# Optimization experiments

Hardware: AMD Instinct MI355X
Metric: run time of the kernel (lower is better)

Reference implementation:

```python
import jax, jax.numpy as jnp
import numpy as np

B, D, U, C = 2048, 512, 512, 100


def setup_inputs() -> dict:
    key = jax.random.key(0)
    k1, k2, k3 = jax.random.split(key, 3)
    x = jax.random.normal(k1, (B, D), dtype=jnp.float32)
    classes = jax.random.randint(k2, (B, 1), 0, C, dtype=jnp.int64)
    # glorot-uniform-like init for the per-class kernel table
    limit = np.sqrt(6.0 / (D + U)).astype(np.float32)
    kernel = jax.random.uniform(k3, (C, D, U), dtype=jnp.float32, minval=-limit, maxval=limit)
    bias = jnp.zeros((C, U), dtype=jnp.float32)
    return {"x": x, "classes": classes, "kernel": kernel, "bias": bias}


def reference(x, classes, kernel, bias):
    cls = jnp.squeeze(classes, axis=1)            # [B]
    w = kernel[cls]                               # [B, D, U] per-sample gathered kernel
    out = jnp.einsum('bd,bdu->bu', x, w)          # batched matmul, x treated as [B,1,D]
    out = out + bias[cls]                         # per-sample gathered bias
    return out                                    # activation is None (linear)
```

## Files before the change

### kernel.cpp

```cpp
#include <hip/hip_runtime.h>
#include <hip/hip_bf16.h>


typedef __attribute__((ext_vector_type(8))) short bf16x8;
typedef __attribute__((ext_vector_type(4))) short short4v;
typedef __attribute__((ext_vector_type(4))) float floatx4;

constexpr int C_CLS   = 100;
constexpr int B_N     = 2048;
constexpr int D_DIM   = 512;
constexpr int U_DIM   = 512;
constexpr int S_CHUNK = 16;
constexpr int MAX_CHUNKS = 228;
constexpr int TU      = 256;
constexpr int PROWS   = 16;
constexpr int PIECES  = D_DIM / PROWS;
constexpr int NWG     = 2 * MAX_CHUNKS;

__device__ __forceinline__ short f2bf(float f) {
    return (short)__builtin_bit_cast(unsigned short, __float2bfloat16(f));
}


__global__ void k_sort(const int* __restrict__ cls, int* __restrict__ order,
                       int* __restrict__ total_chunks, int* __restrict__ chunk_cls,
                       int* __restrict__ chunk_start, int* __restrict__ chunk_len) {
    __shared__ int s_cnt[128], s_off[128], s_chk[128], s_cur[128], s_base[128];
    int tid = threadIdx.x;
    if (tid < 128) s_cnt[tid] = 0;
    __syncthreads();
    for (int i = tid; i < B_N; i += 1024) atomicAdd(&s_cnt[cls[i]], 1);
    __syncthreads();
    int cnt = 0, nch = 0;
    if (tid < 128) {
        cnt = (tid < C_CLS) ? s_cnt[tid] : 0;
        nch = (cnt + S_CHUNK - 1) / S_CHUNK;
        s_off[tid] = cnt; s_chk[tid] = nch;
    }
    __syncthreads();
    for (int st = 1; st < 128; st <<= 1) {
        int a = 0, b = 0;
        if (tid >= st && tid < 128) { a = s_off[tid - st]; b = s_chk[tid - st]; }
        __syncthreads();
        if (tid < 128) { s_off[tid] += a; s_chk[tid] += b; }
        __syncthreads();
    }
    if (tid < C_CLS) {
        int off = s_off[tid] - cnt;
        int cb  = s_chk[tid] - nch;
        s_base[tid] = off;
        s_cur[tid]  = 0;
        for (int j = 0; j < nch; ++j) {
            chunk_cls[cb + j]   = tid;
            chunk_start[cb + j] = off + j * S_CHUNK;
            chunk_len[cb + j]   = min(S_CHUNK, cnt - j * S_CHUNK);
        }
    }
    if (tid == 127) *total_chunks = s_chk[127];
    __syncthreads();
    for (int i = tid; i < B_N; i += 1024) {
        int c = cls[i];
        int p = atomicAdd(&s_cur[c], 1);
        order[s_base[c] + p] = i;
    }
}


#define ISSUE(pi, qq) do {                                                    \
    const int db_ = (pi) * PROWS;                                             \
    _Pragma("unroll")                                                         \
    for (int j_ = 0; j_ < 4; ++j_) {                                          \
        const int r_ = 4 * wv + j_;                                           \
        const float* gp_ = Wg + (size_t)(db_ + r_) * U_DIM + ((lane ^ r_) << 2); \
        __builtin_amdgcn_global_load_lds(                                     \
            (const __attribute__((address_space(1))) void*)gp_,               \
            (__attribute__((address_space(3))) void*)&wbuf[qq][r_][0],        \
            16, 0, 0);                                                        \
    }                                                                         \
} while (0)

#define COMPUTE(pi, qq) do {                                                  \
    const char* xp_ = (const char*)xsb + sA * 1024 +                          \
                      (((pi) * 32 + g4 * 8) ^ sxw_);                          \
    short4v a4 = *reinterpret_cast<const short4v*>(xp_);                      \
    bf16x8 a8;                                                                \
    a8[0] = a4[0]; a8[1] = a4[1]; a8[2] = a4[2]; a8[3] = a4[3];               \
    a8[4] = a4[0]; a8[5] = a4[1]; a8[6] = a4[2]; a8[7] = a4[3];               \
    const char* wb_ = (const char*)wbuf + (qq) * (PROWS * TU * 4);            \
    _Pragma("unroll")                                                         \
    for (int nt = 0; nt < 4; ++nt) {                                          \
        const int cb4_ = ((wv << 6) + nt * 16 + sA) << 2;                     \
        bf16x8 b8;                                                            \
        _Pragma("unroll")                                                     \
        for (int j_ = 0; j_ < 4; ++j_) {                                      \
            const int rl_ = g4 * 4 + j_;                                      \
            float w_ = *reinterpret_cast<const float*>(                       \
                wb_ + rl_ * 1024 + (cb4_ ^ (rl_ << 4)));                      \
            b8[j_] = f2bf(w_);                                                \
        }                                                                     \
        b8[4] = 0; b8[5] = 0; b8[6] = 0; b8[7] = 0;                           \
        acc[nt] = __builtin_amdgcn_mfma_f32_16x16x32_bf16(a8, b8, acc[nt], 0, 0, 0); \
    }                                                                         \
} while (0)

__launch_bounds__(256, 2)
__global__ void k_main(const float* __restrict__ x, const float* __restrict__ kern,
                       const float* __restrict__ bias, const int* __restrict__ order,
                       const int* __restrict__ total_chunks,
                       const int* __restrict__ chunk_cls,
                       const int* __restrict__ chunk_start,
                       const int* __restrict__ chunk_len,
                       float* __restrict__ out) {
    int tc = *total_chunks;
    int A  = 2 * tc;
    int xc = blockIdx.x & 7;
    int ii = blockIdx.x >> 3;
    int q  = A >> 3, r = A & 7;
    int mycnt = (xc < r) ? (q + 1) : q;
    if (ii >= mycnt) return;
    int g = ((xc < r) ? xc * (q + 1) : r * (q + 1) + (xc - r) * q) + ii;

    int chunk = g >> 1;
    int ytile = g & 1;

    int tid  = threadIdx.x;
    int lane = tid & 63;
    int wv   = tid >> 6;
    int sA   = lane & 15;
    int g4   = lane >> 4;
    const int sxw_ = (sA & 7) << 4;

    int c     = chunk_cls[chunk];
    int start = chunk_start[chunk];
    int len   = chunk_len[chunk];
    int u0    = ytile * TU;

    __shared__ float          wbuf[2][PROWS][TU];
    __shared__ unsigned short xsb[S_CHUNK][D_DIM];
    __shared__ int            sidx[S_CHUNK];

    const float* Wg = kern + (size_t)c * (D_DIM * U_DIM) + u0;

    if (tid < S_CHUNK) sidx[tid] = (tid < len) ? order[start + tid] : -1;
    asm volatile("s_waitcnt lgkmcnt(0)" ::: "memory");
    __builtin_amdgcn_s_barrier();

    int srow = tid >> 4;
    int cb   = (tid & 15) * 32;
    int bsmp = sidx[srow]; if (bsmp < 0) bsmp = sidx[0];
    float4 xv[8];
    #pragma unroll
    for (int j = 0; j < 8; ++j)
        xv[j] = reinterpret_cast<const float4*>(x + (size_t)bsmp * D_DIM + cb)[j];

    ISSUE(0, 0);
    ISSUE(1, 1);
    asm volatile("s_waitcnt vmcnt(8)" ::: "memory");

    {
        char* xrow = (char*)xsb + srow * 1024;
        int   swz  = (srow & 7) << 4;
        #pragma unroll
        for (int m = 0; m < 4; ++m) {
            bf16x8 pk;
            pk[0] = f2bf(xv[2*m].x);   pk[1] = f2bf(xv[2*m].y);
            pk[2] = f2bf(xv[2*m].z);   pk[3] = f2bf(xv[2*m].w);
            pk[4] = f2bf(xv[2*m+1].x); pk[5] = f2bf(xv[2*m+1].y);
            pk[6] = f2bf(xv[2*m+1].z); pk[7] = f2bf(xv[2*m+1].w);
            *reinterpret_cast<bf16x8*>(xrow + ((cb * 2 + m * 16) ^ swz)) = pk;
        }
    }
    asm volatile("s_waitcnt lgkmcnt(0)" ::: "memory");
    __builtin_amdgcn_s_barrier();

    floatx4 acc[4];
    #pragma unroll
    for (int k = 0; k < 4; ++k) acc[k] = (floatx4){0.f, 0.f, 0.f, 0.f};

    #pragma unroll 1
    for (int i = 0; i < PIECES; ++i) {
        if (i + 1 < PIECES) asm volatile("s_waitcnt vmcnt(4)" ::: "memory");
        else                asm volatile("s_waitcnt vmcnt(0)" ::: "memory");
        __builtin_amdgcn_s_barrier();
        COMPUTE(i, (i & 1));
        asm volatile("" ::: "memory");
        __builtin_amdgcn_s_barrier();
        if (i + 2 < PIECES) ISSUE(i + 2, (i & 1));
    }

    #pragma unroll
    for (int nt = 0; nt < 4; ++nt) {
        int u = u0 + (wv << 6) + nt * 16 + sA;
        float bb = bias[c * U_DIM + u];
        #pragma unroll
        for (int r2 = 0; r2 < 4; ++r2) {
            int b = sidx[g4 * 4 + r2];
            if (b >= 0) out[(size_t)b * U_DIM + u] = acc[nt][r2] + bb;
        }
    }
}


extern "C" void kernel_launch(void* const* d_in, const int* in_sizes, int n_in,
                              void* d_out, int out_size, void* d_ws, size_t ws_size,
                              hipStream_t stream) {
    const float* x    = (const float*)d_in[0];
    const int*   cls  = (const int*)d_in[1];
    const float* kern = (const float*)d_in[2];
    const float* bias = (const float*)d_in[3];
    float*       out  = (float*)d_out;

    int* ws           = (int*)d_ws;
    int* order        = ws;
    int* total_chunks = ws + 2048;
    int* chunk_cls    = ws + 2112;
    int* chunk_start  = ws + 2368;
    int* chunk_len    = ws + 2624;

    hipLaunchKernelGGL(k_sort, dim3(1), dim3(1024), 0, stream,
                       cls, order, total_chunks, chunk_cls, chunk_start, chunk_len);
    hipLaunchKernelGGL(k_main, dim3(NWG), dim3(256), 0, stream,
                       x, kern, bias, order, total_chunks, chunk_cls, chunk_start, chunk_len, out);
}
```

Before: 38.76 us.

## Use 32-sample chunks with 128-wide U tiles and 4-deep LDS pipeline

Doubles samples per chunk to 32 so each kernel tile loaded from memory feeds two MFMA row-blocks, and halves the U tile to 128 so there are four tiles per chunk. The weight prefetch ring grows from 2 to 4 stages with explicit vmcnt waits unrolled at the tail. The aim is to cut redundant kernel-table reads for classes with more than 16 samples and to hide more load latency. In exchange, small classes waste more padded rows, and the extra x rows are loaded per workgroup.

```diff
diff --git a/kernel.cpp b/kernel.cpp
--- a/kernel.cpp
+++ b/kernel.cpp
@@ -10,12 +10,13 @@
 constexpr int B_N     = 2048;
 constexpr int D_DIM   = 512;
 constexpr int U_DIM   = 512;
-constexpr int S_CHUNK = 16;
-constexpr int MAX_CHUNKS = 228;
-constexpr int TU      = 256;
+constexpr int S_CHUNK = 32;
+constexpr int MAX_CHUNKS = 164;
+constexpr int TU      = 128;
 constexpr int PROWS   = 16;
 constexpr int PIECES  = D_DIM / PROWS;
-constexpr int NWG     = 2 * MAX_CHUNKS;
+constexpr int NQ      = 4;
+constexpr int NWG     = 4 * MAX_CHUNKS;
 
 __device__ __forceinline__ short f2bf(float f) {
     return (short)__builtin_bit_cast(unsigned short, __float2bfloat16(f));
@@ -69,9 +70,11 @@
 #define ISSUE(pi, qq) do {                                                    \
     const int db_ = (pi) * PROWS;                                             \
     _Pragma("unroll")                                                         \
-    for (int j_ = 0; j_ < 4; ++j_) {                                          \
-        const int r_ = 4 * wv + j_;                                           \
-        const float* gp_ = Wg + (size_t)(db_ + r_) * U_DIM + ((lane ^ r_) << 2); \
+    for (int j_ = 0; j_ < 2; ++j_) {                                          \
+        const int r_  = wv * 4 + 2 * j_;           \
+        const int rr_ = r_ + (lane >> 5);        \
+        const float* gp_ = Wg + (size_t)(db_ + rr_) * U_DIM                   \
+                           + (((lane & 31) ^ (rr_ & 15)) << 2);               \
         __builtin_amdgcn_global_load_lds(                                     \
             (const __attribute__((address_space(1))) void*)gp_,               \
             (__attribute__((address_space(3))) void*)&wbuf[qq][r_][0],        \
@@ -80,27 +83,43 @@
 } while (0)
 
 #define COMPUTE(pi, qq) do {                                                  \
-    const char* xp_ = (const char*)xsb + sA * 1024 +                          \
-                      (((pi) * 32 + g4 * 8) ^ sxw_);                          \
-    short4v a4 = *reinterpret_cast<const short4v*>(xp_);                      \
-    bf16x8 a8;                                                                \
-    a8[0] = a4[0]; a8[1] = a4[1]; a8[2] = a4[2]; a8[3] = a4[3];               \
-    a8[4] = a4[0]; a8[5] = a4[1]; a8[6] = a4[2]; a8[7] = a4[3];               \
+    bf16x8 a8_0, a8_1;                                                        \
+    {                                                                         \
+        const int xb_ = ((pi) * 32 + g4 * 8) ^ sxw_;                          \
+        short4v a4 = *reinterpret_cast<const short4v*>(                       \
+            (const char*)xsb + sA * 1024 + xb_);                              \
+        a8_0[0]=a4[0]; a8_0[1]=a4[1]; a8_0[2]=a4[2]; a8_0[3]=a4[3];           \
+        a8_0[4]=a4[0]; a8_0[5]=a4[1]; a8_0[6]=a4[2]; a8_0[7]=a4[3];           \
+        short4v a4b = *reinterpret_cast<const short4v*>(                      \
+            (const char*)xsb + (16 + sA) * 1024 + xb_);                       \
+        a8_1[0]=a4b[0]; a8_1[1]=a4b[1]; a8_1[2]=a4b[2]; a8_1[3]=a4b[3];       \
+        a8_1[4]=a4b[0]; a8_1[5]=a4b[1]; a8_1[6]=a4b[2]; a8_1[7]=a4b[3];       \
+    }                                                                         \
     const char* wb_ = (const char*)wbuf + (qq) * (PROWS * TU * 4);            \
     _Pragma("unroll")                                                         \
-    for (int nt = 0; nt < 4; ++nt) {                                          \
-        const int cb4_ = ((wv << 6) + nt * 16 + sA) << 2;                     \
+    for (int nt = 0; nt < 2; ++nt) {                                          \
+        const int cb4_ = ((wv << 5) + nt * 16 + sA) << 2;                     \
         bf16x8 b8;                                                            \
         _Pragma("unroll")                                                     \
         for (int j_ = 0; j_ < 4; ++j_) {                                      \
             const int rl_ = g4 * 4 + j_;                                      \
             float w_ = *reinterpret_cast<const float*>(                       \
-                wb_ + rl_ * 1024 + (cb4_ ^ (rl_ << 4)));                      \
+                wb_ + rl_ * 512 + (cb4_ ^ (rl_ << 4)));                       \
             b8[j_] = f2bf(w_);                                                \
         }                                                                     \
         b8[4] = 0; b8[5] = 0; b8[6] = 0; b8[7] = 0;                           \
-        acc[nt] = __builtin_amdgcn_mfma_f32_16x16x32_bf16(a8, b8, acc[nt], 0, 0, 0); \
+        acc0[nt] = __builtin_amdgcn_mfma_f32_16x16x32_bf16(a8_0, b8, acc0[nt], 0, 0, 0); \
+        acc1[nt] = __builtin_amdgcn_mfma_f32_16x16x32_bf16(a8_1, b8, acc1[nt], 0, 0, 0); \
     }                                                                         \
+} while (0)
+
+#define STEP(pi, NCNT) do {                                                   \
+    asm volatile("s_waitcnt vmcnt(" #NCNT ")" ::: "memory");                  \
+    __builtin_amdgcn_s_barrier();                  \
+    COMPUTE(pi, (pi) & 3);                                                    \
+    asm volatile("" ::: "memory");                                            \
+    __builtin_amdgcn_s_barrier();               \
+    if ((pi) + NQ < PIECES) ISSUE((pi) + NQ, (pi) & 3);                       \
 } while (0)
 
 __launch_bounds__(256, 2)
@@ -112,7 +131,7 @@
                        const int* __restrict__ chunk_len,
                        float* __restrict__ out) {
     int tc = *total_chunks;
-    int A  = 2 * tc;
+    int A  = 4 * tc;
     int xc = blockIdx.x & 7;
     int ii = blockIdx.x >> 3;
     int q  = A >> 3, r = A & 7;
@@ -120,8 +139,8 @@
     if (ii >= mycnt) return;
     int g = ((xc < r) ? xc * (q + 1) : r * (q + 1) + (xc - r) * q) + ii;
 
-    int chunk = g >> 1;
-    int ytile = g & 1;
+    int chunk = g >> 2;
+    int ytile = g & 3;
 
     int tid  = threadIdx.x;
     int lane = tid & 63;
@@ -135,7 +154,7 @@
     int len   = chunk_len[chunk];
     int u0    = ytile * TU;
 
-    __shared__ float          wbuf[2][PROWS][TU];
+    __shared__ float          wbuf[NQ][PROWS][TU];
     __shared__ unsigned short xsb[S_CHUNK][D_DIM];
     __shared__ int            sidx[S_CHUNK];
 
@@ -145,57 +164,73 @@
     asm volatile("s_waitcnt lgkmcnt(0)" ::: "memory");
     __builtin_amdgcn_s_barrier();
 
-    int srow = tid >> 4;
-    int cb   = (tid & 15) * 32;
-    int bsmp = sidx[srow]; if (bsmp < 0) bsmp = sidx[0];
-    float4 xv[8];
-    #pragma unroll
-    for (int j = 0; j < 8; ++j)
-        xv[j] = reinterpret_cast<const float4*>(x + (size_t)bsmp * D_DIM + cb)[j];
-
+    float4 xv0[8], xv1[8];
+    int srow0 = (tid >> 4), srow1 = 16 + (tid >> 4);
+    int cb    = (tid & 15) * 32;
+    {
+        int b0 = sidx[srow0]; if (b0 < 0) b0 = sidx[0];
+        int b1 = sidx[srow1]; if (b1 < 0) b1 = sidx[0];
+        #pragma unroll
+        for (int j = 0; j < 8; ++j)
+            xv0[j] = reinterpret_cast<const float4*>(x + (size_t)b0 * D_DIM + cb)[j];
+        #pragma unroll
+        for (int j = 0; j < 8; ++j)
+            xv1[j] = reinterpret_cast<const float4*>(x + (size_t)b1 * D_DIM + cb)[j];
+    }
     ISSUE(0, 0);
     ISSUE(1, 1);
+    ISSUE(2, 2);
+    ISSUE(3, 3);
     asm volatile("s_waitcnt vmcnt(8)" ::: "memory");
 
     {
-        char* xrow = (char*)xsb + srow * 1024;
-        int   swz  = (srow & 7) << 4;
-        #pragma unroll
-        for (int m = 0; m < 4; ++m) {
-            bf16x8 pk;
-            pk[0] = f2bf(xv[2*m].x);   pk[1] = f2bf(xv[2*m].y);
-            pk[2] = f2bf(xv[2*m].z);   pk[3] = f2bf(xv[2*m].w);
-            pk[4] = f2bf(xv[2*m+1].x); pk[5] = f2bf(xv[2*m+1].y);
-            pk[6] = f2bf(xv[2*m+1].z); pk[7] = f2bf(xv[2*m+1].w);
-            *reinterpret_cast<bf16x8*>(xrow + ((cb * 2 + m * 16) ^ swz)) = pk;
+        #pragma unroll
+        for (int p = 0; p < 2; ++p) {
+            int   row  = p ? srow1 : srow0;
+            char* xrow = (char*)xsb + row * 1024;
+            int   swz  = (row & 7) << 4;
+            #pragma unroll
+            for (int m = 0; m < 4; ++m) {
+                float4 va = p ? xv1[2*m]     : xv0[2*m];
+                float4 vb = p ? xv1[2*m + 1] : xv0[2*m + 1];
+                bf16x8 pk;
+                pk[0] = f2bf(va.x); pk[1] = f2bf(va.y);
+                pk[2] = f2bf(va.z); pk[3] = f2bf(va.w);
+                pk[4] = f2bf(vb.x); pk[5] = f2bf(vb.y);
+                pk[6] = f2bf(vb.z); pk[7] = f2bf(vb.w);
+                *reinterpret_cast<bf16x8*>(xrow + ((cb * 2 + m * 16) ^ swz)) = pk;
+            }
         }
     }
     asm volatile("s_waitcnt lgkmcnt(0)" ::: "memory");
     __builtin_amdgcn_s_barrier();
 
-    floatx4 acc[4];
+    floatx4 acc0[2], acc1[2];
     #pragma unroll
-    for (int k = 0; k < 4; ++k) acc[k] = (floatx4){0.f, 0.f, 0.f, 0.f};
+    for (int k = 0; k < 2; ++k) {
+        acc0[k] = (floatx4){0.f, 0.f, 0.f, 0.f};
+        acc1[k] = (floatx4){0.f, 0.f, 0.f, 0.f};
+    }
 
     #pragma unroll 1
-    for (int i = 0; i < PIECES; ++i) {
-        if (i + 1 < PIECES) asm volatile("s_waitcnt vmcnt(4)" ::: "memory");
-        else                asm volatile("s_waitcnt vmcnt(0)" ::: "memory");
-        __builtin_amdgcn_s_barrier();
-        COMPUTE(i, (i & 1));
-        asm volatile("" ::: "memory");
-        __builtin_amdgcn_s_barrier();
-        if (i + 2 < PIECES) ISSUE(i + 2, (i & 1));
-    }
+    for (int i = 0; i <= 27; ++i) STEP(i, 6);
+    STEP(28, 6);
+    STEP(29, 4);
+    STEP(30, 2);
+    STEP(31, 0);
 
     #pragma unroll
-    for (int nt = 0; nt < 4; ++nt) {
-        int u = u0 + (wv << 6) + nt * 16 + sA;
-        float bb = bias[c * U_DIM + u];
-        #pragma unroll
-        for (int r2 = 0; r2 < 4; ++r2) {
-            int b = sidx[g4 * 4 + r2];
-            if (b >= 0) out[(size_t)b * U_DIM + u] = acc[nt][r2] + bb;
+    for (int mt = 0; mt < 2; ++mt) {
+        #pragma unroll
+        for (int nt = 0; nt < 2; ++nt) {
+            int u  = u0 + (wv << 5) + nt * 16 + sA;
+            float bb = bias[c * U_DIM + u];
+            floatx4 a = mt ? acc1[nt] : acc0[nt];
+            #pragma unroll
+            for (int r2 = 0; r2 < 4; ++r2) {
+                int b = sidx[mt * 16 + g4 * 4 + r2];
+                if (b >= 0) out[(size_t)b * U_DIM + u] = a[r2] + bb;
+            }
         }
     }
 }
@@ -214,8 +249,8 @@
     int* order        = ws;
     int* total_chunks = ws + 2048;
     int* chunk_cls    = ws + 2112;
-    int* chunk_start  = ws + 2368;
-    int* chunk_len    = ws + 2624;
+    int* chunk_start  = ws + 2304;
+    int* chunk_len    = ws + 2496;
 
     hipLaunchKernelGGL(k_sort, dim3(1), dim3(1024), 0, stream,
                        cls, order, total_chunks, chunk_cls, chunk_start, chunk_len);
```

After: 32.41 us. -16.4%, faster.
